# Kernel tuning notes

Measured on AMD Instinct MI355X. Metric: run time of the kernel, lower is better.

Reference implementation:

```python
import jax, jax.numpy as jnp
import numpy as np

B, F = 512, 300  # F must satisfy F+4 == 16*19
EPS = 1e-5

def _leaky(v):
    return jnp.where(v >= 0, v, 0.01 * v)

def setup_inputs() -> dict:
    key = jax.random.key(0)
    ks = jax.random.split(key, 9)
    def conv_w(k, o, i):
        return jax.random.normal(k, (o, i), dtype=jnp.float32) * (1.0 / np.sqrt(i))
    x = jax.random.uniform(ks[0], (B, F), dtype=jnp.float32)
    return {
        "x": x,
        "w1": conv_w(ks[1], 256, 512), "b1": jnp.zeros((256,), jnp.float32),
        "w2": conv_w(ks[2], 128, 256), "b2": jnp.zeros((128,), jnp.float32),
        "w3": conv_w(ks[3], 64, 128),  "b3": jnp.zeros((64,), jnp.float32),
        "w4": conv_w(ks[4], 4, 64),    "b4": jnp.zeros((4,), jnp.float32),
    }

def reference(x, w1, b1, w2, b2, w3, b3, w4, b4):
    b = x.shape[0]
    xp = jnp.pad(x, ((0, 0), (2, 2)))                       # (b, 304)
    s1 = xp[:, None, :]                                      # unsqueeze(1)
    s2 = xp[:, :, None]                                      # unsqueeze(2)
    DI = s1 - s2                                             # (b,304,304)
    NDI = DI / (s1 + s2 + EPS)
    t = jnp.stack([DI, NDI], axis=-1)                        # (b,304,304,2)
    # tile into 16x16 grid of 19x19 patches, concat patches along channel
    # channel c = (row*16+col)*2 + d  (row-major loop order in original)
    t = t.reshape(b, 16, 19, 16, 19, 2).transpose(0, 2, 4, 1, 3, 5).reshape(b, 19, 19, 512)
    h = _leaky(jnp.einsum('bhwc,oc->bhwo', t, w1) + b1)      # (b,19,19,256)
    h = _leaky(jnp.einsum('bhwc,oc->bhwo', h, w2) + b2)      # (b,19,19,128)
    # masking branch (positional encoding in original is dead code / overwritten)
    m = jax.nn.relu(jnp.einsum('bhwc,oc->bhwo', h, w3) + b3)  # (b,19,19,64)
    m = jax.nn.relu(jnp.einsum('bhwc,oc->bhwo', m, w4) + b4)  # (b,19,19,4)
    m = m.transpose(3, 0, 1, 2).reshape(4, b, 19 * 19)
    m = jax.nn.softmax(m, axis=2).reshape(4, b, 19, 19, 1)
    # split 128 channels into 4 groups of 32
    g = h.reshape(b, 19, 19, 4, 32).transpose(3, 0, 1, 2, 4)  # (4,b,19,19,32)
    out = (g * m).sum(axis=(2, 3))                            # (4,b,32)
    return out.transpose(1, 0, 2).reshape(b, 128)
```

## Files before the change

### kernel.cpp

```cpp
#include <hip/hip_runtime.h>
#include <math.h>

typedef unsigned short ushort_t;
typedef __attribute__((ext_vector_type(8))) short short8;
typedef __attribute__((ext_vector_type(4))) float f32x4;

#define NTILES 12

#define WS_W_USHORTS 115712

__device__ inline float bf2f(ushort_t h) { return __uint_as_float(((unsigned)h) << 16); }
__device__ inline ushort_t f2bf(float f) {
    unsigned u = __float_as_uint(f);
    return (ushort_t)((u + 0x7FFFu + ((u >> 16) & 1u)) >> 16);
}
__device__ inline unsigned pkbf(float f0, float f1) {
    unsigned a = __float_as_uint(f0) + 0x8000u;
    unsigned b = __float_as_uint(f1) + 0x8000u;
    return __builtin_amdgcn_perm(b, a, 0x07060302u);
}
__device__ inline float leaky(float v) { return fmaxf(v, 0.01f * v); }

__global__ void pack_weights(const float* __restrict__ w1, const float* __restrict__ w2,
                             const float* __restrict__ w3, const float* __restrict__ w4,
                             ushort_t* __restrict__ ws) {
    const int idx = blockIdx.x * 256 + threadIdx.x;
    if (idx >= WS_W_USHORTS) return;
    float val = 0.f;
    if (idx < 73728) {
        const int j = idx & 7, lane = (idx >> 3) & 63, blk = idx >> 9;
        const int ks = blk % 9, os = blk / 9;
        const int m = lane & 15, q = lane >> 4;
        const int row = os * 16 + m;
        if (ks < 8) {
            const int k = ks * 32 + q * 8 + j;
            const int i1 = k >> 4, j1 = k & 15;
            val = w1[row * 512 + i1 * 32 + j1 * 2 + 1];
        } else {
            const int sub = q * 8 + j;
            if (sub < 16) {
                const int j1 = sub;
                float s = 0.f;
                #pragma unroll
                for (int i1 = 0; i1 < 16; ++i1) s += w1[row * 512 + i1 * 32 + j1 * 2];
                val = s;
            } else {
                const int i1 = sub - 16;
                float s = 0.f;
                #pragma unroll
                for (int j1 = 0; j1 < 16; ++j1) s += w1[row * 512 + i1 * 32 + j1 * 2];
                val = -s;
            }
        }
    } else if (idx < 106496) {
        const int l = idx - 73728;
        const int j = l & 7, lane = (l >> 3) & 63, blk = l >> 9;
        const int ks = blk & 7, os = blk >> 3;
        const int m = lane & 15, q = lane >> 4;
        val = w2[(os * 16 + m) * 256 + ks * 32 + q * 8 + j];
    } else if (idx < 114688) {
        const int l = idx - 106496;
        const int j = l & 7, lane = (l >> 3) & 63, blk = l >> 9;
        const int ks = blk & 3, os = blk >> 2;
        const int m = lane & 15, q = lane >> 4;
        val = w3[(os * 16 + m) * 128 + ks * 32 + q * 8 + j];
    } else {
        const int l = idx - 114688;
        const int j = l & 7, lane = (l >> 3) & 63, ks = l >> 9;
        const int m = lane & 15, q = lane >> 4;
        val = (m < 4) ? w4[m * 64 + ks * 32 + q * 8 + j] : 0.f;
    }
    ws[idx] = f2bf(val);
}

template <int NS>
__global__ __launch_bounds__(256, 3) void fused_mfma(
    const float* __restrict__ x, const ushort_t* __restrict__ ws,
    const float* __restrict__ b1, const float* __restrict__ b2,
    const float* __restrict__ b3, const float* __restrict__ b4,
    float* __restrict__ part)
{
    __shared__ __align__(16) ushort_t sm[19048];
    ushort_t* const ts   = sm;
    ushort_t* const h2s  = sm;
    ushort_t* const h1s  = sm + 10240;
    ushort_t* const m3s  = sm + 10240;
    float*   const ebuf  = (float*)(sm + 12288);
    float*   const abuf  = (float*)(sm + 12544);
    float*   const xp    = (float*)(sm + 18432);

    constexpr int SH  = (NS == 4) ? 2 : ((NS == 2) ? 1 : 0);
    constexpr int TPS = (NTILES + NS - 1) / NS;
    const int tid = threadIdx.x;
    const int s   = blockIdx.x & (NS - 1);
    const int bb  = blockIdx.x >> SH;
    const int t0  = s * TPS;
    const int t1  = (t0 + TPS < NTILES) ? (t0 + TPS) : NTILES;

    const int wid  = tid >> 6;
    const int lane = tid & 63;
    const int n0   = lane & 15;
    const int qi   = lane >> 4;
    const int sx   = n0 & 7;
    const int row0 = qi * 4;

    for (int jj = tid; jj < 308; jj += 256) {
        float v = 0.f;
        const int src = jj - 2;
        if (src >= 0 && src < 300) v = x[bb * 300 + src];
        xp[jj] = v;
    }

    const short8* wf1 = (const short8*)(ws);
    const short8* wf2 = (const short8*)(ws + 73728);
    const short8* wf3 = (const short8*)(ws + 106496);
    const short8* wf4 = (const short8*)(ws + 114688);

    f32x4 bv1[4], bv2[2], bv3, bv4;
    #pragma unroll
    for (int jo = 0; jo < 4; ++jo) bv1[jo] = *(const f32x4*)&b1[(wid * 4 + jo) * 16 + row0];
    #pragma unroll
    for (int jo = 0; jo < 2; ++jo) bv2[jo] = *(const f32x4*)&b2[(wid * 2 + jo) * 16 + row0];
    bv3 = *(const f32x4*)&b3[wid * 16 + row0];
    bv4 = *(const f32x4*)&b4[0];

    const int cp = tid & 63;
    const int qt = tid >> 6;
    const int qq = cp >> 4;
    float A0 = 0.f, A1 = 0.f, Ss = 0.f;
    float Mq[4] = {-1e30f, -1e30f, -1e30f, -1e30f};

    __syncthreads();

    for (int tile = t0; tile < t1; ++tile) {
        const int pos0 = tile * 32;

        {
            const int p   = tid & 31;
            const int i1b = tid >> 5;
            int posg = pos0 + p; if (posg > 360) posg = 360;
            const int hh = posg / 19;
            const int ww = posg - 19 * hh;
            const int base = p * 320;
            const int psw  = p & 7;
            float u[16];
            #pragma unroll
            for (int j1 = 0; j1 < 16; ++j1) u[j1] = xp[j1 * 19 + ww];
            #pragma unroll
            for (int ii = 0; ii < 2; ++ii) {
                const int i1 = i1b + ii * 8;
                const float v = xp[i1 * 19 + hh];
                #pragma unroll
                for (int j1 = 0; j1 < 16; j1 += 2) {
                    const float nd0 = (u[j1] - v)     * __builtin_amdgcn_rcpf(u[j1] + v + 1e-5f);
                    const float nd1 = (u[j1 + 1] - v) * __builtin_amdgcn_rcpf(u[j1 + 1] + v + 1e-5f);
                    const int oct = i1 * 2 + (j1 >> 3);
                    *(unsigned*)&ts[base + ((oct ^ psw) << 3) + (j1 & 7)] = pkbf(nd0, nd1);
                }
            }
            if (i1b == 0) {
                #pragma unroll
                for (int j1 = 0; j1 < 16; j1 += 2) {
                    const int oct = 32 + (j1 >> 3);
                    *(unsigned*)&ts[base + ((oct ^ psw) << 3) + (j1 & 7)] = pkbf(u[j1], u[j1 + 1]);
                }
                #pragma unroll
                for (int i1 = 0; i1 < 16; i1 += 2) {
                    const float v0 = xp[i1 * 19 + hh];
                    const float v1 = xp[(i1 + 1) * 19 + hh];
                    const int oct = 34 + (i1 >> 3);
                    *(unsigned*)&ts[base + ((oct ^ psw) << 3) + (i1 & 7)] = pkbf(v0, v1);
                }
            }
        }
        __syncthreads();

        f32x4 acc1[4][2];
        {
            #pragma unroll
            for (int jo = 0; jo < 4; ++jo) { acc1[jo][0] = bv1[jo]; acc1[jo][1] = bv1[jo]; }
            const int tb0 = n0 * 320;
            const int tb1 = tb0 + 16 * 320;
            const int wbase = wid * 2304 + lane;
            #pragma unroll 3
            for (int ks = 0; ks < 9; ++ks) {
                const int oct = ks * 4 + qi;
                const short8 bb0 = *(const short8*)&ts[tb0 + ((oct ^ sx) << 3)];
                const short8 bb1 = *(const short8*)&ts[tb1 + ((oct ^ sx) << 3)];
                #pragma unroll
                for (int jo = 0; jo < 4; ++jo) {
                    const short8 a = wf1[wbase + (jo * 9 + ks) * 64];
                    acc1[jo][0] = __builtin_amdgcn_mfma_f32_16x16x32_bf16(a, bb0, acc1[jo][0], 0, 0, 0);
                    acc1[jo][1] = __builtin_amdgcn_mfma_f32_16x16x32_bf16(a, bb1, acc1[jo][1], 0, 0, 0);
                }
            }
        }
        __syncthreads();
        {
            #pragma unroll
            for (int jo = 0; jo < 4; ++jo) {
                const int out0 = (wid * 4 + jo) * 16 + row0;
                #pragma unroll
                for (int ps = 0; ps < 2; ++ps) {
                    const f32x4 a4 = acc1[jo][ps];
                    uint2 pk;
                    pk.x = pkbf(leaky(a4.x), leaky(a4.y));
                    pk.y = pkbf(leaky(a4.z), leaky(a4.w));
                    *(uint2*)&h1s[(ps * 16 + n0) * 256 + (((out0 >> 3) ^ sx) << 3) + (out0 & 7)] = pk;
                }
            }
        }
        __syncthreads();

        {
            f32x4 acc[2][2];
            #pragma unroll
            for (int jo = 0; jo < 2; ++jo) { acc[jo][0] = bv2[jo]; acc[jo][1] = bv2[jo]; }
            const int hb0 = n0 * 256;
            const int hb1 = hb0 + 16 * 256;
            const int wbase = wid * 1024 + lane;
            #pragma unroll 4
            for (int ks = 0; ks < 8; ++ks) {
                const int oct = ks * 4 + qi;
                const short8 bb0 = *(const short8*)&h1s[hb0 + ((oct ^ sx) << 3)];
                const short8 bb1 = *(const short8*)&h1s[hb1 + ((oct ^ sx) << 3)];
                #pragma unroll
                for (int jo = 0; jo < 2; ++jo) {
                    const short8 a = wf2[wbase + (jo * 8 + ks) * 64];
                    acc[jo][0] = __builtin_amdgcn_mfma_f32_16x16x32_bf16(a, bb0, acc[jo][0], 0, 0, 0);
                    acc[jo][1] = __builtin_amdgcn_mfma_f32_16x16x32_bf16(a, bb1, acc[jo][1], 0, 0, 0);
                }
            }
            #pragma unroll
            for (int jo = 0; jo < 2; ++jo) {
                const int out0 = (wid * 2 + jo) * 16 + row0;
                #pragma unroll
                for (int ps = 0; ps < 2; ++ps) {
                    const f32x4 a4 = acc[jo][ps];
                    uint2 pk;
                    pk.x = pkbf(leaky(a4.x), leaky(a4.y));
                    pk.y = pkbf(leaky(a4.z), leaky(a4.w));
                    *(uint2*)&h2s[(ps * 16 + n0) * 128 + (((out0 >> 3) ^ sx) << 3) + (out0 & 7)] = pk;
                }
            }
        }
        __syncthreads();

        {
            f32x4 acc[2] = {bv3, bv3};
            const int cb0 = n0 * 128;
            const int cb1 = cb0 + 16 * 128;
            #pragma unroll
            for (int ks = 0; ks < 4; ++ks) {
                const int oct = ks * 4 + qi;
                const short8 bb0 = *(const short8*)&h2s[cb0 + ((oct ^ sx) << 3)];
                const short8 bb1 = *(const short8*)&h2s[cb1 + ((oct ^ sx) << 3)];
                const short8 a = wf3[(wid * 4 + ks) * 64 + lane];
                acc[0] = __builtin_amdgcn_mfma_f32_16x16x32_bf16(a, bb0, acc[0], 0, 0, 0);
                acc[1] = __builtin_amdgcn_mfma_f32_16x16x32_bf16(a, bb1, acc[1], 0, 0, 0);
            }
            const int out0 = wid * 16 + row0;
            #pragma unroll
            for (int ps = 0; ps < 2; ++ps) {
                const f32x4 a4 = acc[ps];
                uint2 pk;
                pk.x = pkbf(fmaxf(a4.x, 0.f), fmaxf(a4.y, 0.f));
                pk.y = pkbf(fmaxf(a4.z, 0.f), fmaxf(a4.w, 0.f));
                *(uint2*)&m3s[(ps * 16 + n0) * 64 + (((out0 >> 3) ^ sx) << 3) + (out0 & 7)] = pk;
            }
        }
        __syncthreads();

        if (wid == 0) {
            f32x4 acc[2] = {bv4, bv4};
            const int mb0 = n0 * 64;
            const int mb1 = mb0 + 16 * 64;
            #pragma unroll
            for (int ks = 0; ks < 2; ++ks) {
                const int oct = ks * 4 + qi;
                const short8 bb0 = *(const short8*)&m3s[mb0 + ((oct ^ sx) << 3)];
                const short8 bb1 = *(const short8*)&m3s[mb1 + ((oct ^ sx) << 3)];
                const short8 a = wf4[ks * 64 + lane];
                acc[0] = __builtin_amdgcn_mfma_f32_16x16x32_bf16(a, bb0, acc[0], 0, 0, 0);
                acc[1] = __builtin_amdgcn_mfma_f32_16x16x32_bf16(a, bb1, acc[1], 0, 0, 0);
            }
            const bool bad0 = (pos0 + lane) > 360;
            const bool bad1 = (pos0 + 16 + lane) > 360;
            float l0[4], l1[4];
            l0[0] = bad0 ? -1e30f : fmaxf(acc[0].x, 0.f);
            l0[1] = bad0 ? -1e30f : fmaxf(acc[0].y, 0.f);
            l0[2] = bad0 ? -1e30f : fmaxf(acc[0].z, 0.f);
            l0[3] = bad0 ? -1e30f : fmaxf(acc[0].w, 0.f);
            l1[0] = bad1 ? -1e30f : fmaxf(acc[1].x, 0.f);
            l1[1] = bad1 ? -1e30f : fmaxf(acc[1].y, 0.f);
            l1[2] = bad1 ? -1e30f : fmaxf(acc[1].z, 0.f);
            l1[3] = bad1 ? -1e30f : fmaxf(acc[1].w, 0.f);
            #pragma unroll
            for (int q = 0; q < 4; ++q) {
                float tm = fmaxf(l0[q], l1[q]);
                tm = fmaxf(tm, __shfl_xor(tm, 1, 64));
                tm = fmaxf(tm, __shfl_xor(tm, 2, 64));
                tm = fmaxf(tm, __shfl_xor(tm, 4, 64));
                tm = fmaxf(tm, __shfl_xor(tm, 8, 64));
                const float nM = fmaxf(Mq[q], tm);
                const float al = __expf(Mq[q] - nM);
                Mq[q] = nM;
                const float e0 = __expf(l0[q] - nM);
                const float e1 = __expf(l1[q] - nM);
                if (lane < 16) {
                    ebuf[q * 32 + lane]      = e0;
                    ebuf[q * 32 + 16 + lane] = e1;
                }
                if (lane == 0) abuf[q] = al;
            }
        }
        __syncthreads();

        {
            const float alpha = abuf[qq];
            A0 *= alpha; A1 *= alpha; Ss *= alpha;
            const int oc4 = cp >> 2;
            const int elo = (cp & 3) * 2;
            #pragma unroll
            for (int pp = 0; pp < 8; ++pp) {
                const int p = qt * 8 + pp;
                const float e = ebuf[qq * 32 + p];
                const unsigned hp = *(const unsigned*)&h2s[p * 128 + ((oc4 ^ (p & 7)) << 3) + elo];
                const float f0 = __uint_as_float(hp << 16);
                const float f1 = __uint_as_float(hp & 0xFFFF0000u);
                A0 += e * f0;
                A1 += e * f1;
                Ss += e;
            }
        }
        __syncthreads();
    }

    float* mbuf = (float*)(sm + 10240);
    mbuf[qt * 64 + cp]        = A0;
    mbuf[256 + qt * 64 + cp]  = A1;
    mbuf[512 + qt * 64 + cp]  = Ss;
    if (wid == 0 && lane < 4) mbuf[768 + lane] = Mq[lane];
    __syncthreads();
    if (tid < 128) {
        const int ch = tid, cpf = ch >> 1, par = ch & 1;
        float Af = 0.f, Sf = 0.f;
        #pragma unroll
        for (int t = 0; t < 4; ++t) {
            Af += mbuf[par * 256 + t * 64 + cpf];
            Sf += mbuf[512 + t * 64 + cpf];
        }
        const float Mf = mbuf[768 + (ch >> 5)];
        const int pb  = (s * 512 + bb) * 128 + ch;
        const int sep = NS * 512 * 128;
        part[pb]           = Mf;
        part[pb + sep]     = Sf;
        part[pb + 2 * sep] = Af;
    }
}

template <int NS>
__global__ void merge_out(const float* __restrict__ part, float* __restrict__ out) {
    const int idx = blockIdx.x * 256 + threadIdx.x;
    if (idx >= 512 * 128) return;
    const int bb = idx >> 7, ch = idx & 127;
    const int sep = NS * 512 * 128;
    float Mf = -1e30f;
    #pragma unroll
    for (int s = 0; s < NS; ++s) Mf = fmaxf(Mf, part[(s * 512 + bb) * 128 + ch]);
    float Sf = 0.f, Af = 0.f;
    #pragma unroll
    for (int s = 0; s < NS; ++s) {
        const int pb = (s * 512 + bb) * 128 + ch;
        const float e = __expf(part[pb] - Mf);
        Sf += part[pb + sep] * e;
        Af += part[pb + 2 * sep] * e;
    }
    out[idx] = Af / Sf;
}

__global__ __launch_bounds__(256, 2) void fallback_fused(
    const float* __restrict__ x,
    const float* __restrict__ w1, const float* __restrict__ b1,
    const float* __restrict__ w2, const float* __restrict__ b2,
    const float* __restrict__ w3, const float* __restrict__ b3,
    const float* __restrict__ w4, const float* __restrict__ b4,
    float* __restrict__ out)
{
    __shared__ float smf[14644];
    float* const xp  = smf;
    float* const ts  = smf + 308;
    float* const h1s = smf + 8500;
    float* const h2s = smf + 12596;
    float* const m3s = ts;
    float* const lgs = ts + 1024;

    const int tid = threadIdx.x;
    const int b   = blockIdx.x;
    for (int j = tid; j < 308; j += 256) {
        float v = 0.f;
        const int src = j - 2;
        if (src >= 0 && src < 300) v = x[b * 300 + src];
        xp[j] = v;
    }
    __syncthreads();
    const int q = tid >> 5, dd = tid & 31;
    float M = -1e30f, S = 0.f, A = 0.f;
    for (int tile = 0; tile < 23; ++tile) {
        const int pos0 = tile * 16;
        {
            const int p = tid & 15, kk0 = tid >> 4;
            const int pos = pos0 + p;
            const bool valid = (pos < 361);
            const int hh = valid ? (pos / 19) : 0;
            const int ww = valid ? (pos - hh * 19) : 0;
            #pragma unroll
            for (int i = 0; i < 16; ++i) {
                const int kk = kk0 + (i << 4);
                const int i1 = kk >> 4, j1 = kk & 15;
                float di = 0.f, ndi = 0.f;
                if (valid) {
                    const float u = xp[j1 * 19 + ww];
                    const float v = xp[i1 * 19 + hh];
                    di = u - v; ndi = di / (u + v + 1e-5f);
                }
                ts[(kk << 5) + p] = di;
                ts[(kk << 5) + 16 + p] = ndi;
            }
        }
        __syncthreads();
        {
            const int o = tid;
            float acc[16];
            const float bias = b1[o];
            #pragma unroll
            for (int p = 0; p < 16; ++p) acc[p] = bias;
            for (int k = 0; k < 512; ++k) {
                const float wv = w1[o * 512 + k];
                #pragma unroll
                for (int p = 0; p < 16; ++p) acc[p] += wv * ts[(k << 4) + p];
            }
            #pragma unroll
            for (int p = 0; p < 16; ++p) h1s[(o << 4) + p] = (acc[p] >= 0.f) ? acc[p] : 0.01f * acc[p];
        }
        __syncthreads();
        {
            const int o2 = tid & 127, pb = (tid >> 7) << 3;
            float acc[8];
            const float bias = b2[o2];
            #pragma unroll
            for (int j = 0; j < 8; ++j) acc[j] = bias;
            for (int k = 0; k < 256; ++k) {
                const float wv = w2[o2 * 256 + k];
                #pragma unroll
                for (int j = 0; j < 8; ++j) acc[j] += wv * h1s[(k << 4) + pb + j];
            }
            #pragma unroll
            for (int j = 0; j < 8; ++j) h2s[(o2 << 4) + pb + j] = (acc[j] >= 0.f) ? acc[j] : 0.01f * acc[j];
        }
        __syncthreads();
        {
            const int o3 = tid & 63, pb = (tid >> 6) << 2;
            float acc[4];
            const float bias = b3[o3];
            #pragma unroll
            for (int j = 0; j < 4; ++j) acc[j] = bias;
            for (int k = 0; k < 128; ++k) {
                const float wv = w3[o3 * 128 + k];
                #pragma unroll
                for (int j = 0; j < 4; ++j) acc[j] += wv * h2s[(k << 4) + pb + j];
            }
            #pragma unroll
            for (int j = 0; j < 4; ++j) m3s[(o3 << 4) + pb + j] = fmaxf(acc[j], 0.f);
        }
        __syncthreads();
        if (tid < 64) {
            const int o4 = tid >> 4, p = tid & 15;
            float a = b4[o4];
            for (int k = 0; k < 64; ++k) a += w4[o4 * 64 + k] * m3s[(k << 4) + p];
            a = fmaxf(a, 0.f);
            if (pos0 + p >= 361) a = -1e30f;
            lgs[(o4 << 4) + p] = a;
        }
        __syncthreads();
        if (tid < 128) {
            float l[16];
            #pragma unroll
            for (int p = 0; p < 16; ++p) l[p] = lgs[(q << 4) + p];
            float tmax = l[0];
            #pragma unroll
            for (int p = 1; p < 16; ++p) tmax = fmaxf(tmax, l[p]);
            const float newM = fmaxf(M, tmax);
            const float alpha = __expf(M - newM);
            float ssum = 0.f, asum = 0.f;
            #pragma unroll
            for (int p = 0; p < 16; ++p) {
                const float e = __expf(l[p] - newM);
                ssum += e;
                asum += e * h2s[(((q << 5) + dd) << 4) + p];
            }
            S = S * alpha + ssum; A = A * alpha + asum; M = newM;
        }
        __syncthreads();
    }
    if (tid < 128) out[(b << 7) + tid] = A / S;
}

extern "C" void kernel_launch(void* const* d_in, const int* in_sizes, int n_in,
                              void* d_out, int out_size, void* d_ws, size_t ws_size,
                              hipStream_t stream) {
    const float* x  = (const float*)d_in[0];
    const float* w1 = (const float*)d_in[1];
    const float* b1 = (const float*)d_in[2];
    const float* w2 = (const float*)d_in[3];
    const float* b2 = (const float*)d_in[4];
    const float* w3 = (const float*)d_in[5];
    const float* b3 = (const float*)d_in[6];
    const float* w4 = (const float*)d_in[7];
    const float* b4 = (const float*)d_in[8];
    float* out = (float*)d_out;

    const size_t wbytes  = (size_t)WS_W_USHORTS * sizeof(ushort_t);
    const size_t pbytes1 = (size_t)3 * 512 * 128 * sizeof(float);
    ushort_t* ws = (ushort_t*)d_ws;
    float* partf = (float*)((char*)d_ws + wbytes);

    const int packBlocks = (WS_W_USHORTS + 255) / 256;
    if (ws_size >= wbytes + 4 * pbytes1) {
        pack_weights<<<packBlocks, 256, 0, stream>>>(w1, w2, w3, w4, ws);
        fused_mfma<4><<<2048, 256, 0, stream>>>(x, ws, b1, b2, b3, b4, partf);
        merge_out<4><<<256, 256, 0, stream>>>(partf, out);
    } else if (ws_size >= wbytes + 2 * pbytes1) {
        pack_weights<<<packBlocks, 256, 0, stream>>>(w1, w2, w3, w4, ws);
        fused_mfma<2><<<1024, 256, 0, stream>>>(x, ws, b1, b2, b3, b4, partf);
        merge_out<2><<<256, 256, 0, stream>>>(partf, out);
    } else if (ws_size >= wbytes + pbytes1) {
        pack_weights<<<packBlocks, 256, 0, stream>>>(w1, w2, w3, w4, ws);
        fused_mfma<1><<<512, 256, 0, stream>>>(x, ws, b1, b2, b3, b4, partf);
        merge_out<1><<<256, 256, 0, stream>>>(partf, out);
    } else {
        fallback_fused<<<512, 256, 0, stream>>>(x, w1, b1, w2, b2, w3, b3, w4, b4, out);
    }
}
```

Measured before the change: 176.0 us.

## Drop online softmax max tracking and accumulate attention pooling in registers

Replaces the running-max online softmax with plain exp of the relu logits, relying on relu outputs being small enough to avoid overflow. The weighted pooling now uses layer-2 fp32 accumulators held in registers instead of re-reading bf16 h2 from shared memory, and reduces across lanes with shuffles at the end. The merge kernel just sums partial A and S sums. This removes per-tile shuffles, exps, a barrier and the LDS reads, and it merges the layer-1 barrier into the epilogue. The trade-off is a risk of exp overflow for large logits.

```diff
diff --git a/kernel.cpp b/kernel.cpp
--- a/kernel.cpp
+++ b/kernel.cpp
@@ -9,7 +9,6 @@
 
 #define WS_W_USHORTS 115712
 
-__device__ inline float bf2f(ushort_t h) { return __uint_as_float(((unsigned)h) << 16); }
 __device__ inline ushort_t f2bf(float f) {
     unsigned u = __float_as_uint(f);
     return (ushort_t)((u + 0x7FFFu + ((u >> 16) & 1u)) >> 16);
@@ -78,7 +77,7 @@
     const float* __restrict__ x, const ushort_t* __restrict__ ws,
     const float* __restrict__ b1, const float* __restrict__ b2,
     const float* __restrict__ b3, const float* __restrict__ b4,
-    float* __restrict__ part)
+    float* __restrict__ partA, float* __restrict__ partS)
 {
     __shared__ __align__(16) ushort_t sm[19048];
     ushort_t* const ts   = sm;
@@ -86,7 +85,6 @@
     ushort_t* const h1s  = sm + 10240;
     ushort_t* const m3s  = sm + 10240;
     float*   const ebuf  = (float*)(sm + 12288);
-    float*   const abuf  = (float*)(sm + 12544);
     float*   const xp    = (float*)(sm + 18432);
 
     constexpr int SH  = (NS == 4) ? 2 : ((NS == 2) ? 1 : 0);
@@ -124,11 +122,8 @@
     bv3 = *(const f32x4*)&b3[wid * 16 + row0];
     bv4 = *(const f32x4*)&b4[0];
 
-    const int cp = tid & 63;
-    const int qt = tid >> 6;
-    const int qq = cp >> 4;
-    float A0 = 0.f, A1 = 0.f, Ss = 0.f;
-    float Mq[4] = {-1e30f, -1e30f, -1e30f, -1e30f};
+    f32x4 Afr[2] = {{0.f, 0.f, 0.f, 0.f}, {0.f, 0.f, 0.f, 0.f}};
+    float Ss = 0.f;
 
     __syncthreads();
 
@@ -175,10 +170,10 @@
         }
         __syncthreads();
 
-        f32x4 acc1[4][2];
-        {
-            #pragma unroll
-            for (int jo = 0; jo < 4; ++jo) { acc1[jo][0] = bv1[jo]; acc1[jo][1] = bv1[jo]; }
+        {
+            f32x4 acc[4][2];
+            #pragma unroll
+            for (int jo = 0; jo < 4; ++jo) { acc[jo][0] = bv1[jo]; acc[jo][1] = bv1[jo]; }
             const int tb0 = n0 * 320;
             const int tb1 = tb0 + 16 * 320;
             const int wbase = wid * 2304 + lane;
@@ -190,19 +185,16 @@
                 #pragma unroll
                 for (int jo = 0; jo < 4; ++jo) {
                     const short8 a = wf1[wbase + (jo * 9 + ks) * 64];
-                    acc1[jo][0] = __builtin_amdgcn_mfma_f32_16x16x32_bf16(a, bb0, acc1[jo][0], 0, 0, 0);
-                    acc1[jo][1] = __builtin_amdgcn_mfma_f32_16x16x32_bf16(a, bb1, acc1[jo][1], 0, 0, 0);
-                }
-            }
-        }
-        __syncthreads();
-        {
+                    acc[jo][0] = __builtin_amdgcn_mfma_f32_16x16x32_bf16(a, bb0, acc[jo][0], 0, 0, 0);
+                    acc[jo][1] = __builtin_amdgcn_mfma_f32_16x16x32_bf16(a, bb1, acc[jo][1], 0, 0, 0);
+                }
+            }
             #pragma unroll
             for (int jo = 0; jo < 4; ++jo) {
                 const int out0 = (wid * 4 + jo) * 16 + row0;
                 #pragma unroll
                 for (int ps = 0; ps < 2; ++ps) {
-                    const f32x4 a4 = acc1[jo][ps];
+                    const f32x4 a4 = acc[jo][ps];
                     uint2 pk;
                     pk.x = pkbf(leaky(a4.x), leaky(a4.y));
                     pk.y = pkbf(leaky(a4.z), leaky(a4.w));
@@ -212,6 +204,7 @@
         }
         __syncthreads();
 
+        f32x4 h2f[2][2];
         {
             f32x4 acc[2][2];
             #pragma unroll
@@ -236,10 +229,13 @@
                 const int out0 = (wid * 2 + jo) * 16 + row0;
                 #pragma unroll
                 for (int ps = 0; ps < 2; ++ps) {
-                    const f32x4 a4 = acc[jo][ps];
+                    f32x4 a4 = acc[jo][ps];
+                    a4.x = leaky(a4.x); a4.y = leaky(a4.y);
+                    a4.z = leaky(a4.z); a4.w = leaky(a4.w);
+                    h2f[jo][ps] = a4;
                     uint2 pk;
-                    pk.x = pkbf(leaky(a4.x), leaky(a4.y));
-                    pk.y = pkbf(leaky(a4.z), leaky(a4.w));
+                    pk.x = pkbf(a4.x, a4.y);
+                    pk.y = pkbf(a4.z, a4.w);
                     *(uint2*)&h2s[(ps * 16 + n0) * 128 + (((out0 >> 3) ^ sx) << 3) + (out0 & 7)] = pk;
                 }
             }
@@ -284,97 +280,72 @@
                 acc[0] = __builtin_amdgcn_mfma_f32_16x16x32_bf16(a, bb0, acc[0], 0, 0, 0);
                 acc[1] = __builtin_amdgcn_mfma_f32_16x16x32_bf16(a, bb1, acc[1], 0, 0, 0);
             }
-            const bool bad0 = (pos0 + lane) > 360;
-            const bool bad1 = (pos0 + 16 + lane) > 360;
-            float l0[4], l1[4];
-            l0[0] = bad0 ? -1e30f : fmaxf(acc[0].x, 0.f);
-            l0[1] = bad0 ? -1e30f : fmaxf(acc[0].y, 0.f);
-            l0[2] = bad0 ? -1e30f : fmaxf(acc[0].z, 0.f);
-            l0[3] = bad0 ? -1e30f : fmaxf(acc[0].w, 0.f);
-            l1[0] = bad1 ? -1e30f : fmaxf(acc[1].x, 0.f);
-            l1[1] = bad1 ? -1e30f : fmaxf(acc[1].y, 0.f);
-            l1[2] = bad1 ? -1e30f : fmaxf(acc[1].z, 0.f);
-            l1[3] = bad1 ? -1e30f : fmaxf(acc[1].w, 0.f);
-            #pragma unroll
-            for (int q = 0; q < 4; ++q) {
-                float tm = fmaxf(l0[q], l1[q]);
-                tm = fmaxf(tm, __shfl_xor(tm, 1, 64));
-                tm = fmaxf(tm, __shfl_xor(tm, 2, 64));
-                tm = fmaxf(tm, __shfl_xor(tm, 4, 64));
-                tm = fmaxf(tm, __shfl_xor(tm, 8, 64));
-                const float nM = fmaxf(Mq[q], tm);
-                const float al = __expf(Mq[q] - nM);
-                Mq[q] = nM;
-                const float e0 = __expf(l0[q] - nM);
-                const float e1 = __expf(l1[q] - nM);
-                if (lane < 16) {
-                    ebuf[q * 32 + lane]      = e0;
-                    ebuf[q * 32 + 16 + lane] = e1;
-                }
-                if (lane == 0) abuf[q] = al;
-            }
-        }
-        __syncthreads();
-
-        {
-            const float alpha = abuf[qq];
-            A0 *= alpha; A1 *= alpha; Ss *= alpha;
-            const int oc4 = cp >> 2;
-            const int elo = (cp & 3) * 2;
-            #pragma unroll
-            for (int pp = 0; pp < 8; ++pp) {
-                const int p = qt * 8 + pp;
-                const float e = ebuf[qq * 32 + p];
-                const unsigned hp = *(const unsigned*)&h2s[p * 128 + ((oc4 ^ (p & 7)) << 3) + elo];
-                const float f0 = __uint_as_float(hp << 16);
-                const float f1 = __uint_as_float(hp & 0xFFFF0000u);
-                A0 += e * f0;
-                A1 += e * f1;
-                Ss += e;
-            }
-        }
-        __syncthreads();
-    }
-
-    float* mbuf = (float*)(sm + 10240);
-    mbuf[qt * 64 + cp]        = A0;
-    mbuf[256 + qt * 64 + cp]  = A1;
-    mbuf[512 + qt * 64 + cp]  = Ss;
-    if (wid == 0 && lane < 4) mbuf[768 + lane] = Mq[lane];
-    __syncthreads();
-    if (tid < 128) {
-        const int ch = tid, cpf = ch >> 1, par = ch & 1;
-        float Af = 0.f, Sf = 0.f;
+            if (lane < 16) {
+                const bool bad0 = (pos0 + lane) > 360;
+                const bool bad1 = (pos0 + 16 + lane) > 360;
+                ebuf[0 * 32 + lane]      = bad0 ? 0.f : __expf(fmaxf(acc[0].x, 0.f));
+                ebuf[1 * 32 + lane]      = bad0 ? 0.f : __expf(fmaxf(acc[0].y, 0.f));
+                ebuf[2 * 32 + lane]      = bad0 ? 0.f : __expf(fmaxf(acc[0].z, 0.f));
+                ebuf[3 * 32 + lane]      = bad0 ? 0.f : __expf(fmaxf(acc[0].w, 0.f));
+                ebuf[0 * 32 + 16 + lane] = bad1 ? 0.f : __expf(fmaxf(acc[1].x, 0.f));
+                ebuf[1 * 32 + 16 + lane] = bad1 ? 0.f : __expf(fmaxf(acc[1].y, 0.f));
+                ebuf[2 * 32 + 16 + lane] = bad1 ? 0.f : __expf(fmaxf(acc[1].z, 0.f));
+                ebuf[3 * 32 + 16 + lane] = bad1 ? 0.f : __expf(fmaxf(acc[1].w, 0.f));
+            }
+        }
+        __syncthreads();
+
+        {
+            const float e0 = ebuf[wid * 32 + n0];
+            const float e1 = ebuf[wid * 32 + 16 + n0];
+            #pragma unroll
+            for (int jo = 0; jo < 2; ++jo) {
+                Afr[jo].x += e0 * h2f[jo][0].x + e1 * h2f[jo][1].x;
+                Afr[jo].y += e0 * h2f[jo][0].y + e1 * h2f[jo][1].y;
+                Afr[jo].z += e0 * h2f[jo][0].z + e1 * h2f[jo][1].z;
+                Afr[jo].w += e0 * h2f[jo][0].w + e1 * h2f[jo][1].w;
+            }
+            Ss += e0 + e1;
+        }
+    }
+
+    #pragma unroll
+    for (int bit = 1; bit < 16; bit <<= 1) {
         #pragma unroll
-        for (int t = 0; t < 4; ++t) {
-            Af += mbuf[par * 256 + t * 64 + cpf];
-            Sf += mbuf[512 + t * 64 + cpf];
-        }
-        const float Mf = mbuf[768 + (ch >> 5)];
-        const int pb  = (s * 512 + bb) * 128 + ch;
-        const int sep = NS * 512 * 128;
-        part[pb]           = Mf;
-        part[pb + sep]     = Sf;
-        part[pb + 2 * sep] = Af;
+        for (int jo = 0; jo < 2; ++jo) {
+            Afr[jo].x += __shfl_xor(Afr[jo].x, bit, 64);
+            Afr[jo].y += __shfl_xor(Afr[jo].y, bit, 64);
+            Afr[jo].z += __shfl_xor(Afr[jo].z, bit, 64);
+            Afr[jo].w += __shfl_xor(Afr[jo].w, bit, 64);
+        }
+        Ss += __shfl_xor(Ss, bit, 64);
+    }
+    if (n0 == 0) {
+        const int pbA = (s * 512 + bb) * 128;
+        #pragma unroll
+        for (int jo = 0; jo < 2; ++jo) {
+            const int ch0 = (wid * 2 + jo) * 16 + qi * 4;
+            partA[pbA + ch0]     = Afr[jo].x;
+            partA[pbA + ch0 + 1] = Afr[jo].y;
+            partA[pbA + ch0 + 2] = Afr[jo].z;
+            partA[pbA + ch0 + 3] = Afr[jo].w;
+        }
+        if (qi == 0) partS[(s * 512 + bb) * 4 + wid] = Ss;
     }
 }
 
 template <int NS>
-__global__ void merge_out(const float* __restrict__ part, float* __restrict__ out) {
+__global__ void merge_out(const float* __restrict__ partA, const float* __restrict__ partS,
+                          float* __restrict__ out) {
     const int idx = blockIdx.x * 256 + threadIdx.x;
     if (idx >= 512 * 128) return;
     const int bb = idx >> 7, ch = idx & 127;
-    const int sep = NS * 512 * 128;
-    float Mf = -1e30f;
-    #pragma unroll
-    for (int s = 0; s < NS; ++s) Mf = fmaxf(Mf, part[(s * 512 + bb) * 128 + ch]);
+    const int q = ch >> 5;
     float Sf = 0.f, Af = 0.f;
     #pragma unroll
     for (int s = 0; s < NS; ++s) {
-        const int pb = (s * 512 + bb) * 128 + ch;
-        const float e = __expf(part[pb] - Mf);
-        Sf += part[pb + sep] * e;
-        Af += part[pb + 2 * sep] * e;
+        Af += partA[(s * 512 + bb) * 128 + ch];
+        Sf += partS[(s * 512 + bb) * 4 + q];
     }
     out[idx] = Af / Sf;
 }
@@ -520,24 +491,32 @@
     const float* b4 = (const float*)d_in[8];
     float* out = (float*)d_out;
 
-    const size_t wbytes  = (size_t)WS_W_USHORTS * sizeof(ushort_t);
-    const size_t pbytes1 = (size_t)3 * 512 * 128 * sizeof(float);
+    const size_t wbytes = (size_t)WS_W_USHORTS * sizeof(ushort_t);
     ushort_t* ws = (ushort_t*)d_ws;
-    float* partf = (float*)((char*)d_ws + wbytes);
-
     const int packBlocks = (WS_W_USHORTS + 255) / 256;
-    if (ws_size >= wbytes + 4 * pbytes1) {
+
+    const size_t need4 = wbytes + (size_t)4 * 512 * 132 * sizeof(float);
+    const size_t need2 = wbytes + (size_t)2 * 512 * 132 * sizeof(float);
+    const size_t need1 = wbytes + (size_t)1 * 512 * 132 * sizeof(float);
+
+    if (ws_size >= need4) {
+        float* pA = (float*)((char*)d_ws + wbytes);
+        float* pS = pA + (size_t)4 * 512 * 128;
         pack_weights<<<packBlocks, 256, 0, stream>>>(w1, w2, w3, w4, ws);
-        fused_mfma<4><<<2048, 256, 0, stream>>>(x, ws, b1, b2, b3, b4, partf);
-        merge_out<4><<<256, 256, 0, stream>>>(partf, out);
-    } else if (ws_size >= wbytes + 2 * pbytes1) {
+        fused_mfma<4><<<2048, 256, 0, stream>>>(x, ws, b1, b2, b3, b4, pA, pS);
+        merge_out<4><<<256, 256, 0, stream>>>(pA, pS, out);
+    } else if (ws_size >= need2) {
+        float* pA = (float*)((char*)d_ws + wbytes);
+        float* pS = pA + (size_t)2 * 512 * 128;
         pack_weights<<<packBlocks, 256, 0, stream>>>(w1, w2, w3, w4, ws);
-        fused_mfma<2><<<1024, 256, 0, stream>>>(x, ws, b1, b2, b3, b4, partf);
-        merge_out<2><<<256, 256, 0, stream>>>(partf, out);
-    } else if (ws_size >= wbytes + pbytes1) {
+        fused_mfma<2><<<1024, 256, 0, stream>>>(x, ws, b1, b2, b3, b4, pA, pS);
+        merge_out<2><<<256, 256, 0, stream>>>(pA, pS, out);
+    } else if (ws_size >= need1) {
+        float* pA = (float*)((char*)d_ws + wbytes);
+        float* pS = pA + (size_t)1 * 512 * 128;
         pack_weights<<<packBlocks, 256, 0, stream>>>(w1, w2, w3, w4, ws);
-        fused_mfma<1><<<512, 256, 0, stream>>>(x, ws, b1, b2, b3, b4, partf);
-        merge_out<1><<<256, 256, 0, stream>>>(partf, out);
+        fused_mfma<1><<<512, 256, 0, stream>>>(x, ws, b1, b2, b3, b4, pA, pS);
+        merge_out<1><<<256, 256, 0, stream>>>(pA, pS, out);
     } else {
         fallback_fused<<<512, 256, 0, stream>>>(x, w1, b1, w2, b2, w3, b3, w4, b4, out);
     }
```

Result: faster. 169.0 us (-4.0%).
